# Kernel tuning notes

Measured on AMD Instinct MI355X. Metric: run time of the kernel, lower is better.

Reference implementation:

```python
import jax, jax.numpy as jnp
import numpy as np

N, E, D_IN, D_E, H, OUT, L = 16384, 131072, 128, 64, 256, 16, 4
EPS_MSG = 1e-7   # GENConv message epsilon
EPS_SM = 1e-16   # PyG softmax denominator epsilon


def _ln(x, g, b, eps=1e-5):
    mu = x.mean(-1, keepdims=True)
    var = x.var(-1, keepdims=True)
    return (x - mu) * jax.lax.rsqrt(var + eps) * g + b


def _genconv(x, src, dst, e, w1, b1, lng, lnb, w2, b2, t):
    # message: relu(x_j + edge_attr) + eps  -> [E, H]
    msg = jax.nn.relu(x[src] + e) + EPS_MSG
    # learnable-temperature segment softmax over incoming edges, per feature
    m = msg * t
    mx = jax.ops.segment_max(m, dst, num_segments=N)
    mx = jnp.where(jnp.isfinite(mx), mx, 0.0)  # empty segments -> 0
    ex = jnp.exp(m - mx[dst])
    den = jax.ops.segment_sum(ex, dst, num_segments=N)
    alpha = ex / (den[dst] + EPS_SM)
    agg = jax.ops.segment_sum(msg * alpha, dst, num_segments=N)  # [N, H]
    # root residual then 2-layer MLP: Linear -> LayerNorm -> ReLU -> Linear
    out = agg + x
    h = jax.nn.relu(_ln(out @ w1 + b1, lng, lnb))
    return h @ w2 + b2


def setup_inputs() -> dict:
    key = jax.random.key(0)
    ks = jax.random.split(key, 10)
    gl = lambda k, shape, fan: jax.random.normal(k, shape, jnp.float32) / np.sqrt(fan).astype(np.float32)
    return {
        "x": jax.random.normal(ks[0], (N, D_IN), jnp.float32),
        "edge_index": jax.random.randint(ks[1], (2, E), 0, N, dtype=jnp.int32),
        "edge_attr": jax.random.normal(ks[2], (E, D_E), jnp.float32),
        "enc_w": gl(ks[3], (D_IN, H), D_IN), "enc_b": jnp.zeros((H,), jnp.float32),
        "ee_w": gl(ks[4], (D_E, H), D_E), "ee_b": jnp.zeros((H,), jnp.float32),
        "w1": gl(ks[5], (L, H, 2 * H), H), "b1": jnp.zeros((L, 2 * H), jnp.float32),
        "lng": jnp.ones((L, 2 * H), jnp.float32), "lnb": jnp.zeros((L, 2 * H), jnp.float32),
        "w2": gl(ks[6], (L, 2 * H, H), 2 * H), "b2": jnp.zeros((L, H), jnp.float32),
        "t": jnp.ones((L,), jnp.float32),
        "ng": jnp.ones((L, H), jnp.float32), "nb": jnp.zeros((L, H), jnp.float32),
        "lin_w": gl(ks[7], (H, OUT), H), "lin_b": jnp.zeros((OUT,), jnp.float32),
    }


def reference(x, edge_index, edge_attr, enc_w, enc_b, ee_w, ee_b,
              w1, b1, lng, lnb, w2, b2, t, ng, nb, lin_w, lin_b):
    src, dst = edge_index[0], edge_index[1]
    h = x @ enc_w + enc_b                      # node encoder
    e = edge_attr @ ee_w + ee_b                # edge encoder
    # first layer: conv only (per source forward)
    h = _genconv(h, src, dst, e, w1[0], b1[0], lng[0], lnb[0], w2[0], b2[0], t[0])
    # remaining layers: res+ block = x + conv(relu(norm(x)))  (dropout off in eval)
    for i in range(1, L):
        z = jax.nn.relu(_ln(h, ng[i], nb[i]))
        h = h + _genconv(z, src, dst, e, w1[i], b1[i], lng[i], lnb[i], w2[i], b2[i], t[i])
    h = jax.nn.relu(_ln(h, ng[0], nb[0]))      # layers[0].act(layers[0].norm(x))
    return h @ lin_w + lin_b
```

## Files before the change

kernel.cpp:

```cpp
#include <hip/hip_runtime.h>
#include <stdint.h>
#include <math.h>


typedef __bf16 bf16x8 __attribute__((ext_vector_type(8)));
typedef __bf16 bf16x4 __attribute__((ext_vector_type(4)));
typedef float  f32x4  __attribute__((ext_vector_type(4)));

constexpr int NN   = 16384;
constexpr int NE   = 131072;
constexpr int DIN  = 128;
constexpr int DE   = 64;
constexpr int HD   = 256;
constexpr int HD2  = 512;

__device__ __forceinline__ void gl_lds16(const __bf16* g, __bf16* l) {
  __builtin_amdgcn_global_load_lds((const __attribute__((address_space(1))) void*)g,
                                   (__attribute__((address_space(3))) void*)l, 16, 0, 0);
}

__global__ __launch_bounds__(1024) void k_scan(const int* __restrict__ deg,
                                               int* __restrict__ row_start) {
  __shared__ int part[1024];
  const int t = threadIdx.x;
  const int base = t * 16;
  int loc[16];
  int s = 0;
  #pragma unroll
  for (int i = 0; i < 16; i++) { loc[i] = s; s += deg[base + i]; }
  part[t] = s;
  __syncthreads();
  for (int off = 1; off < 1024; off <<= 1) {
    int v = (t >= off) ? part[t - off] : 0;
    __syncthreads();
    part[t] += v;
    __syncthreads();
  }
  const int excl = (t == 0) ? 0 : part[t - 1];
  #pragma unroll
  for (int i = 0; i < 16; i++) row_start[base + i] = excl + loc[i];
}

__global__ void k_scatter(const int* __restrict__ src, const int* __restrict__ dst,
                          const int* __restrict__ row_start, int* __restrict__ cursor,
                          int2* __restrict__ csr_es) {
  int e = blockIdx.x * 256 + threadIdx.x;
  if (e >= NE) return;
  const int d = dst[e];
  const int p = atomicAdd(&cursor[d], 1);
  csr_es[row_start[d] + p] = make_int2(e, src[e]);
}

__global__ __launch_bounds__(256)
void k_sortw(const int* __restrict__ row_start, const int* __restrict__ deg,
             int2* __restrict__ csr_es, int* __restrict__ posmap) {
  const int wv   = threadIdx.x >> 6;
  const int lane = threadIdx.x & 63;
  const int node = blockIdx.x * 4 + wv;
  if (node >= NN) return;
  const int st = __builtin_amdgcn_readfirstlane(row_start[node]);
  const int dg = __builtin_amdgcn_readfirstlane(deg[node]);
  if (dg <= 1) {
    if (dg == 1 && lane == 0) posmap[csr_es[st].x] = st;
    return;
  }
  if (dg <= 64) {
    int2 pr = make_int2(0x7fffffff, 0);
    if (lane < dg) pr = csr_es[st + lane];
    int rank = 0;
    for (int j = 0; j < dg; j++) {
      const int ej = __builtin_amdgcn_readlane(pr.x, j);
      if (lane < dg && ej < pr.x) rank++;
    }
    if (lane < dg) {
      csr_es[st + rank] = pr;
      posmap[pr.x] = st + rank;
    }
  } else if (lane == 0) {
    for (int a = 1; a < dg; a++) {
      int2 k = csr_es[st + a];
      int b = a - 1;
      while (b >= 0 && csr_es[st + b].x > k.x) { csr_es[st + b + 1] = csr_es[st + b]; b--; }
      csr_es[st + b + 1] = k;
    }
    for (int a = 0; a < dg; a++) posmap[csr_es[st + a].x] = st + a;
  }
}

__global__ void k_prep(const float* __restrict__ enc_w, const float* __restrict__ ee_w,
                       const float* __restrict__ w1, const float* __restrict__ w2,
                       const int* __restrict__ dst, int* __restrict__ deg,
                       __bf16* __restrict__ enc_wT, __bf16* __restrict__ ee_wT,
                       __bf16* __restrict__ w1T, __bf16* __restrict__ w2T) {
  int i = blockIdx.x * 256 + threadIdx.x;
  const int S0 = DIN * HD, S1 = DE * HD, S2 = 4 * HD * HD2, S3 = 4 * HD2 * HD;
  if (i < S0) { int k = i / HD, n = i % HD; enc_wT[n * DIN + k] = (__bf16)enc_w[i]; return; }
  i -= S0;
  if (i < S1) { int k = i / HD, n = i % HD; ee_wT[n * DE + k] = (__bf16)ee_w[i]; return; }
  i -= S1;
  if (i < S2) {
    int l = i / (HD * HD2), r = i % (HD * HD2), k = r / HD2, n = r % HD2;
    w1T[(size_t)l * HD * HD2 + (size_t)n * HD + k] = (__bf16)w1[i]; return;
  }
  i -= S2;
  if (i < S3) {
    int l = i / (HD2 * HD), r = i % (HD2 * HD), k = r / HD, n = r % HD;
    w2T[(size_t)l * HD2 * HD + (size_t)n * HD2 + k] = (__bf16)w2[i]; return;
  }
  i -= S3;
  if (i < NE) { atomicAdd(&deg[dst[i]], 1); return; }
}

template <int RES, int OBF, int STATS, int ESCAT, int AF32>
__global__ __launch_bounds__(256, 3)
void k_gemm(const void* __restrict__ Ap, const __bf16* __restrict__ BT,
            const float* __restrict__ bias, const float* __restrict__ R,
            float* __restrict__ Cf, __bf16* __restrict__ Cb,
            const int* __restrict__ posmap, float2* __restrict__ pstats,
            int M, int Nn, int K) {
  __shared__ __attribute__((aligned(16))) char smem[49152];
  float (*sm)[129] = (float(*)[129])smem;
  float* sbias     = (float*)(smem + 16512);
  float2 (*pst4)[32] = (float2(*)[32])(smem + 17024);
  const __bf16* Ab = (const __bf16*)Ap;
  const float*  Af = (const float*)Ap;
  const int tid  = threadIdx.x;
  const int lane = tid & 63;
  const int wave = tid >> 6;
  const int ntn  = Nn >> 7;
  const int bid  = (int)blockIdx.x;
  const int bn   = (bid >> 3) % ntn;
  const int bm   = (bid & 7) + ((bid >> 3) / ntn) * 8;
  const size_t row0 = (size_t)bm * 128, col0 = (size_t)bn * 128;
  const int wr = (wave >> 1) * 64, wc = (wave & 1) * 64;
  const int ks = lane >> 4, fr = lane & 15;

  auto bufA = [&](int i) -> __bf16* { return (__bf16*)(smem + i * 8192); };
  auto bufB = [&](int i) -> __bf16* { return (__bf16*)(smem + 24576 + i * 8192); };

  f32x4 acc[4][4] = {};

  const int arow = tid >> 2;
  const int aksg = (tid & 3) ^ ((arow >> 1) & 3);

  auto stageB = [&](__bf16* lb, int k0) {
    gl_lds16(BT + (col0 + arow) * K + k0 + aksg * 8, &lb[tid * 8]);
    gl_lds16(BT + (col0 + arow + 64) * K + k0 + aksg * 8, &lb[(tid + 256) * 8]);
  };
  auto stageA = [&](__bf16* la, int k0) {
    gl_lds16(Ab + (row0 + arow) * K + k0 + aksg * 8, &la[tid * 8]);
    gl_lds16(Ab + (row0 + arow + 64) * K + k0 + aksg * 8, &la[(tid + 256) * 8]);
  };
  float4 p0, p1, q0, q1;
  auto loadAf = [&](int k0) {
    const float* a0p = &Af[(row0 + arow) * K + k0 + aksg * 8];
    const float* a1p = &Af[(row0 + arow + 64) * K + k0 + aksg * 8];
    p0 = *(const float4*)a0p; p1 = *(const float4*)(a0p + 4);
    q0 = *(const float4*)a1p; q1 = *(const float4*)(a1p + 4);
  };
  auto writeAf = [&](__bf16* la) {
    bf16x8 o0, o1;
    o0[0] = (__bf16)p0.x; o0[1] = (__bf16)p0.y; o0[2] = (__bf16)p0.z; o0[3] = (__bf16)p0.w;
    o0[4] = (__bf16)p1.x; o0[5] = (__bf16)p1.y; o0[6] = (__bf16)p1.z; o0[7] = (__bf16)p1.w;
    o1[0] = (__bf16)q0.x; o1[1] = (__bf16)q0.y; o1[2] = (__bf16)q0.z; o1[3] = (__bf16)q0.w;
    o1[4] = (__bf16)q1.x; o1[5] = (__bf16)q1.y; o1[6] = (__bf16)q1.z; o1[7] = (__bf16)q1.w;
    *(bf16x8*)&la[tid * 8] = o0;
    *(bf16x8*)&la[(tid + 256) * 8] = o1;
  };

  int slA[4], slB[4];
  #pragma unroll
  for (int m = 0; m < 4; m++) {
    const int rm = wr + m * 16 + fr;
    slA[m] = rm * 4 + (ks ^ ((rm >> 1) & 3));
    const int cn = wc + m * 16 + fr;
    slB[m] = cn * 4 + (ks ^ ((cn >> 1) & 3));
  }

  const int nk = K / 32;
  if (AF32) { loadAf(0); stageB(bufB(0), 0); writeAf(bufA(0)); }
  else      { stageA(bufA(0), 0); stageB(bufB(0), 0); }
  if (nk > 1) {
    if (AF32) { loadAf(32); stageB(bufB(1), 32); writeAf(bufA(1)); }
    else      { stageA(bufA(1), 32); stageB(bufB(1), 32); }
  }
  for (int t = 0; t < nk; t++) {
    const int rem = nk - 1 - t;
    const int nb3 = (t + 2) % 3;
    if (rem >= 2) {
      if (AF32) { loadAf((t + 2) * 32); stageB(bufB(nb3), (t + 2) * 32); }
      else      { stageA(bufA(nb3), (t + 2) * 32); stageB(bufB(nb3), (t + 2) * 32); }
    }
    if (AF32) {
      if (rem >= 2)      asm volatile("s_waitcnt vmcnt(8) lgkmcnt(0)" ::: "memory");
      else if (rem == 1) asm volatile("s_waitcnt vmcnt(2) lgkmcnt(0)" ::: "memory");
      else               asm volatile("s_waitcnt vmcnt(0) lgkmcnt(0)" ::: "memory");
    } else {
      if (rem >= 2)      asm volatile("s_waitcnt vmcnt(8)" ::: "memory");
      else if (rem == 1) asm volatile("s_waitcnt vmcnt(4)" ::: "memory");
      else               asm volatile("s_waitcnt vmcnt(0)" ::: "memory");
    }
    __builtin_amdgcn_s_barrier();
    __builtin_amdgcn_sched_barrier(0);
    const __bf16* la = bufA(t % 3);
    const __bf16* lb = bufB(t % 3);
    bf16x8 af[4], bfr[4];
    #pragma unroll
    for (int m = 0; m < 4; m++) af[m]  = *(const bf16x8*)&la[slA[m] * 8];
    #pragma unroll
    for (int n = 0; n < 4; n++) bfr[n] = *(const bf16x8*)&lb[slB[n] * 8];
    #pragma unroll
    for (int m = 0; m < 4; m++)
      #pragma unroll
      for (int n = 0; n < 4; n++)
        acc[m][n] = __builtin_amdgcn_mfma_f32_16x16x32_bf16(af[m], bfr[n], acc[m][n], 0, 0, 0);
    if (AF32 && rem >= 2) writeAf(bufA(nb3));
    __builtin_amdgcn_s_barrier();
  }
  __syncthreads();

  if (tid < 128) sbias[tid] = bias[col0 + tid];
  const int rbase = (wave >> 1) * 16 + ks * 4;
  const int rr = tid >> 3, cs = (tid & 7) * 16;
  #pragma unroll
  for (int m = 0; m < 4; m++) {
    if (m) __syncthreads();
    #pragma unroll
    for (int n = 0; n < 4; n++)
      #pragma unroll
      for (int r = 0; r < 4; r++)
        sm[rbase + r][wc + n * 16 + fr] = acc[m][n][r];
    __syncthreads();
    const size_t lrow = ((rr & 16) ? 64 : 0) + m * 16 + (rr & 15);
    const size_t grow = row0 + lrow;
    float v[16];
    #pragma unroll
    for (int j = 0; j < 16; j++) v[j] = sm[rr][cs + j] + sbias[cs + j];
    if (STATS) {
      float ssum = 0.f, ssq = 0.f;
      #pragma unroll
      for (int j = 0; j < 16; j++) { ssum += v[j]; ssq += v[j] * v[j]; }
      #pragma unroll
      for (int o = 1; o < 8; o <<= 1) {
        ssum += __shfl_xor(ssum, o);
        ssq  += __shfl_xor(ssq, o);
      }
      if ((tid & 7) == 0) pst4[m][rr].x = ssum, pst4[m][rr].y = ssq;
    }
    const size_t gbase = grow * Nn + col0 + cs;
    if (RES) {
      #pragma unroll
      for (int j = 0; j < 16; j += 4) {
        const float4 rv = *(const float4*)&R[gbase + j];
        v[j] += rv.x; v[j + 1] += rv.y; v[j + 2] += rv.z; v[j + 3] += rv.w;
      }
    }
    if (OBF == 0 || OBF == 2) {
      #pragma unroll
      for (int j = 0; j < 16; j += 4) {
        float4 o; o.x = v[j]; o.y = v[j + 1]; o.z = v[j + 2]; o.w = v[j + 3];
        *(float4*)&Cf[gbase + j] = o;
      }
    }
    if (OBF == 1 || OBF == 2) {
      const size_t crow = ESCAT ? (size_t)posmap[grow] : grow;
      const size_t cbase = crow * Nn + col0 + cs;
      bf16x8 o0, o1;
      #pragma unroll
      for (int j = 0; j < 8; j++) { o0[j] = (__bf16)v[j]; o1[j] = (__bf16)v[8 + j]; }
      *(bf16x8*)&Cb[cbase] = o0;
      *(bf16x8*)&Cb[cbase + 8] = o1;
    }
  }
  if (STATS) {
    __syncthreads();
    if (tid < 128) {
      const int lr = tid;
      const int hi = lr >> 6, m2 = (lr >> 4) & 3, rl = lr & 15;
      pstats[(row0 + lr) * ntn + bn] = pst4[m2][(hi << 4) | rl];
    }
  }
}

template <int RES, int WH>
__global__ __launch_bounds__(256, 2)
void k_mlp(const __bf16* __restrict__ a1, const __bf16* __restrict__ w1T,
           const float* __restrict__ b1v, const float* __restrict__ g1,
           const float* __restrict__ bln1, const __bf16* __restrict__ w2T,
           const float* __restrict__ b2v, const float* __restrict__ R,
           const float* __restrict__ g2, const float* __restrict__ bln2,
           float* __restrict__ hout, __bf16* __restrict__ zout) {
  __shared__ __attribute__((aligned(16))) char smem[60928];
  float* sg1    = (float*)smem;
  float* sb1    = (float*)(smem + 2048);
  float* sbias1 = (float*)(smem + 4096);
  float* sg2    = (float*)(smem + 6144);
  float* sb2    = (float*)(smem + 7168);
  float* sbias2 = (float*)(smem + 8192);
  float2* wred  = (float2*)(smem + 9216);
  float2* lnrow = (float2*)(smem + 10240);
  __bf16* a1t   = (__bf16*)(smem + 10496);
  __bf16* a2t   = (__bf16*)(smem + 26880);
  float (*sm)[264] = (float(*)[264])(smem + 26880);

  const int tid = threadIdx.x, lane = tid & 63, wave = tid >> 6;
  const size_t row0 = (size_t)blockIdx.x * 32;
  const int ks = lane >> 4, fr = lane & 15;

  sg1[tid] = g1[tid];     sg1[tid + 256] = g1[tid + 256];
  sb1[tid] = bln1[tid];   sb1[tid + 256] = bln1[tid + 256];
  sbias1[tid] = b1v[tid]; sbias1[tid + 256] = b1v[tid + 256];
  sg2[tid] = g2[tid]; sb2[tid] = bln2[tid]; sbias2[tid] = b2v[tid];

  #pragma unroll
  for (int j = 0; j < 4; j++) {
    const int s = j * 256 + tid;
    const int r = s >> 5;
    const int cl = (s & 31) ^ (r & 31);
    gl_lds16(a1 + (row0 + r) * HD + cl * 8, &a1t[s * 8]);
  }
  __syncthreads();

  f32x4 acc1[2][8] = {};
  {
    auto loadB1 = [&](int t, bf16x8* b) {
      const int k0 = t * 32;
      #pragma unroll
      for (int n = 0; n < 8; n++) {
        const int col = wave * 128 + n * 16 + fr;
        b[n] = *(const bf16x8*)&w1T[(size_t)col * HD + k0 + ks * 8];
      }
    };
    bf16x8 bA[8], bB[8];
    loadB1(0, bA);
    #pragma unroll
    for (int t = 0; t < 8; t++) {
      bf16x8* bc = (t & 1) ? bB : bA;
      bf16x8* bn = (t & 1) ? bA : bB;
      if (t + 1 < 8) loadB1(t + 1, bn);
      bf16x8 af[2];
      #pragma unroll
      for (int m = 0; m < 2; m++) {
        const int rm = m * 16 + fr;
        af[m] = *(const bf16x8*)&a1t[(rm * 32 + ((4 * t + ks) ^ (rm & 31))) * 8];
      }
      #pragma unroll
      for (int m = 0; m < 2; m++)
        #pragma unroll
        for (int n = 0; n < 8; n++)
          acc1[m][n] = __builtin_amdgcn_mfma_f32_16x16x32_bf16(af[m], bc[n], acc1[m][n], 0, 0, 0);
    }
  }
  #pragma unroll
  for (int m = 0; m < 2; m++)
    #pragma unroll
    for (int n = 0; n < 8; n++) {
      const int col = wave * 128 + n * 16 + fr;
      const float bv = sbias1[col];
      #pragma unroll
      for (int r = 0; r < 4; r++) acc1[m][n][r] += bv;
    }
  #pragma unroll
  for (int m = 0; m < 2; m++)
    #pragma unroll
    for (int r = 0; r < 4; r++) {
      float s = 0.f, q = 0.f;
      #pragma unroll
      for (int n = 0; n < 8; n++) { const float v = acc1[m][n][r]; s += v; q += v * v; }
      #pragma unroll
      for (int o = 1; o < 16; o <<= 1) { s += __shfl_xor(s, o); q += __shfl_xor(q, o); }
      if (fr == 0) {
        const int row = m * 16 + ks * 4 + r;
        wred[wave * 32 + row].x = s;
        wred[wave * 32 + row].y = q;
      }
    }
  __syncthreads();
  if (tid < 32) {
    float s = 0.f, q = 0.f;
    #pragma unroll
    for (int w = 0; w < 4; w++) { s += wred[w * 32 + tid].x; q += wred[w * 32 + tid].y; }
    const float mu = s * (1.f / HD2);
    lnrow[tid].x = mu;
    lnrow[tid].y = rsqrtf(q * (1.f / HD2) - mu * mu + 1e-5f);
  }
  __syncthreads();
  #pragma unroll
  for (int m = 0; m < 2; m++)
    #pragma unroll
    for (int r = 0; r < 4; r++) {
      const int row = m * 16 + ks * 4 + r;
      const float mu = lnrow[row].x, iv = lnrow[row].y;
      #pragma unroll
      for (int n = 0; n < 8; n++) {
        const int col = wave * 128 + n * 16 + fr;
        const float f = (acc1[m][n][r] - mu) * iv * sg1[col] + sb1[col];
        const int chunk = col >> 3, sub = col & 7;
        a2t[(row * 64 + (chunk ^ (row & 63))) * 8 + sub] = (__bf16)fmaxf(f, 0.f);
      }
    }
  __syncthreads();

  f32x4 acc2[2][4] = {};
  {
    auto loadB2 = [&](int t, bf16x8* b) {
      const int k0 = t * 32;
      #pragma unroll
      for (int n = 0; n < 4; n++) {
        const int col = wave * 64 + n * 16 + fr;
        b[n] = *(const bf16x8*)&w2T[(size_t)col * HD2 + k0 + ks * 8];
      }
    };
    bf16x8 bA[4], bB[4];
    loadB2(0, bA);
    #pragma unroll
    for (int t = 0; t < 16; t++) {
      bf16x8* bc = (t & 1) ? bB : bA;
      bf16x8* bn = (t & 1) ? bA : bB;
      if (t + 1 < 16) loadB2(t + 1, bn);
      bf16x8 af[2];
      #pragma unroll
      for (int m = 0; m < 2; m++) {
        const int rm = m * 16 + fr;
        af[m] = *(const bf16x8*)&a2t[(rm * 64 + ((4 * t + ks) ^ (rm & 63))) * 8];
      }
      #pragma unroll
      for (int m = 0; m < 2; m++)
        #pragma unroll
        for (int n = 0; n < 4; n++)
          acc2[m][n] = __builtin_amdgcn_mfma_f32_16x16x32_bf16(af[m], bc[n], acc2[m][n], 0, 0, 0);
    }
  }
  __syncthreads();

  #pragma unroll
  for (int m = 0; m < 2; m++)
    #pragma unroll
    for (int n = 0; n < 4; n++)
      #pragma unroll
      for (int r = 0; r < 4; r++)
        sm[m * 16 + ks * 4 + r][wave * 64 + n * 16 + fr] = acc2[m][n][r];
  __syncthreads();
  const int rr = tid >> 3, c0 = (tid & 7) * 4;
  float v[32];
  float s = 0.f, sq = 0.f;
  #pragma unroll
  for (int j = 0; j < 8; j++) {
    const int c = c0 + j * 32;
    float x0 = sm[rr][c]     + sbias2[c];
    float x1 = sm[rr][c + 1] + sbias2[c + 1];
    float x2 = sm[rr][c + 2] + sbias2[c + 2];
    float x3 = sm[rr][c + 3] + sbias2[c + 3];
    if (RES) {
      const float4 rv = *(const float4*)&R[(row0 + rr) * HD + c];
      x0 += rv.x; x1 += rv.y; x2 += rv.z; x3 += rv.w;
    }
    v[j * 4] = x0; v[j * 4 + 1] = x1; v[j * 4 + 2] = x2; v[j * 4 + 3] = x3;
    s += x0 + x1 + x2 + x3;
    sq += x0 * x0 + x1 * x1 + x2 * x2 + x3 * x3;
  }
  #pragma unroll
  for (int o = 1; o < 8; o <<= 1) { s += __shfl_xor(s, o); sq += __shfl_xor(sq, o); }
  const float mu = s * (1.f / HD);
  const float inv = rsqrtf(sq * (1.f / HD) - mu * mu + 1e-5f);
  #pragma unroll
  for (int j = 0; j < 8; j++) {
    const int c = c0 + j * 32;
    if (WH) {
      float4 o;
      o.x = v[j * 4]; o.y = v[j * 4 + 1]; o.z = v[j * 4 + 2]; o.w = v[j * 4 + 3];
      *(float4*)&hout[(row0 + rr) * HD + c] = o;
    }
    bf16x4 z;
    z[0] = (__bf16)fmaxf((v[j * 4]     - mu) * inv * sg2[c]     + sb2[c],     0.f);
    z[1] = (__bf16)fmaxf((v[j * 4 + 1] - mu) * inv * sg2[c + 1] + sb2[c + 1], 0.f);
    z[2] = (__bf16)fmaxf((v[j * 4 + 2] - mu) * inv * sg2[c + 2] + sb2[c + 2], 0.f);
    z[3] = (__bf16)fmaxf((v[j * 4 + 3] - mu) * inv * sg2[c + 3] + sb2[c + 3], 0.f);
    *(bf16x4*)&zout[(row0 + rr) * HD + c] = z;
  }
}

__global__ __launch_bounds__(256)
void k_msg(const __bf16* __restrict__ zb, const __bf16* __restrict__ ecsr,
           const int* __restrict__ row_start, const int* __restrict__ deg,
           const int2* __restrict__ csr_es, const float* __restrict__ tvec,
           int layer, __bf16* __restrict__ a1) {
  const int wv   = __builtin_amdgcn_readfirstlane(threadIdx.x >> 6);
  const int lane = threadIdx.x & 63;
  const int node = blockIdx.x * 4 + wv;
  const int st = __builtin_amdgcn_readfirstlane(row_start[node]);
  const int dg = __builtin_amdgcn_readfirstlane(deg[node]);
  const float t = tvec[layer];
  const int f0 = lane * 4;

  int my_src = 0;
  if (lane < dg) my_src = csr_es[st + lane].y;
  const bf16x4 sv = *(const bf16x4*)&zb[(size_t)node * HD + f0];

  float den[4] = {0.f, 0.f, 0.f, 0.f}, agg[4] = {0.f, 0.f, 0.f, 0.f};
  const int dmain = dg < 64 ? dg : 64;
  int j = 0;
  for (; j + 8 <= dmain; j += 8) {
    bf16x4 zv[8], ev[8];
    #pragma unroll
    for (int u = 0; u < 8; u++) {
      const int sn = __builtin_amdgcn_readlane(my_src, j + u);
      zv[u] = *(const bf16x4*)&zb[(size_t)sn * HD + f0];
      ev[u] = *(const bf16x4*)&ecsr[(size_t)(st + j + u) * HD + f0];
    }
    #pragma unroll
    for (int u = 0; u < 8; u++)
      #pragma unroll
      for (int q = 0; q < 4; q++) {
        const float m  = fmaxf((float)zv[u][q] + (float)ev[u][q], 0.f) + 1e-7f;
        const float ex = __expf(m * t);
        den[q] += ex;
        agg[q] += m * ex;
      }
  }
  for (; j + 4 <= dmain; j += 4) {
    bf16x4 zv[4], ev[4];
    #pragma unroll
    for (int u = 0; u < 4; u++) {
      const int sn = __builtin_amdgcn_readlane(my_src, j + u);
      zv[u] = *(const bf16x4*)&zb[(size_t)sn * HD + f0];
      ev[u] = *(const bf16x4*)&ecsr[(size_t)(st + j + u) * HD + f0];
    }
    #pragma unroll
    for (int u = 0; u < 4; u++)
      #pragma unroll
      for (int q = 0; q < 4; q++) {
        const float m  = fmaxf((float)zv[u][q] + (float)ev[u][q], 0.f) + 1e-7f;
        const float ex = __expf(m * t);
        den[q] += ex;
        agg[q] += m * ex;
      }
  }
  for (; j < dmain; j++) {
    const int sn = __builtin_amdgcn_readlane(my_src, j);
    const bf16x4 zv = *(const bf16x4*)&zb[(size_t)sn * HD + f0];
    const bf16x4 ev = *(const bf16x4*)&ecsr[(size_t)(st + j) * HD + f0];
    #pragma unroll
    for (int q = 0; q < 4; q++) {
      const float m  = fmaxf((float)zv[q] + (float)ev[q], 0.f) + 1e-7f;
      const float ex = __expf(m * t);
      den[q] += ex;
      agg[q] += m * ex;
    }
  }
  for (int jj = 64; jj < dg; jj++) {
    const int2 pr = csr_es[st + jj];
    const bf16x4 zv = *(const bf16x4*)&zb[(size_t)pr.y * HD + f0];
    const bf16x4 ev = *(const bf16x4*)&ecsr[(size_t)(st + jj) * HD + f0];
    #pragma unroll
    for (int q = 0; q < 4; q++) {
      const float m  = fmaxf((float)zv[q] + (float)ev[q], 0.f) + 1e-7f;
      const float ex = __expf(m * t);
      den[q] += ex;
      agg[q] += m * ex;
    }
  }
  bf16x4 r;
  #pragma unroll
  for (int q = 0; q < 4; q++) {
    const float res = (dg > 0) ? agg[q] / (den[q] + 1e-16f) : 0.f;
    r[q] = (__bf16)(res + (float)sv[q]);
  }
  *(bf16x4*)&a1[(size_t)node * HD + f0] = r;
}

__global__ __launch_bounds__(256)
void k_head(const __bf16* __restrict__ zb, const float* __restrict__ lw,
            const float* __restrict__ lb, float* __restrict__ out) {
  __shared__ float slw[256 * 16];
  __shared__ __bf16 srow[16 * 256];
  const int t = threadIdx.x;
  const size_t row0 = (size_t)blockIdx.x * 16;
  #pragma unroll
  for (int j = 0; j < 16; j++) slw[j * 256 + t] = lw[j * 256 + t];
  #pragma unroll
  for (int j = 0; j < 2; j++) {
    const int c = j * 256 + t;
    ((bf16x8*)srow)[c] = ((const bf16x8*)(zb + row0 * 256))[c];
  }
  __syncthreads();
  const int rl = t >> 4, col = t & 15;
  float s = lb[col];
  for (int k0 = 0; k0 < 256; k0 += 8) {
    const bf16x8 zv = *(const bf16x8*)&srow[rl * 256 + k0];
    #pragma unroll
    for (int q = 0; q < 8; q++) s += (float)zv[q] * slw[(k0 + q) * 16 + col];
  }
  out[(row0 + rl) * 16 + col] = s;
}

extern "C" void kernel_launch(void* const* d_in, const int* in_sizes, int n_in,
                              void* d_out, int out_size, void* d_ws, size_t ws_size,
                              hipStream_t stream) {
  const float* x     = (const float*)d_in[0];
  const int*   ei    = (const int*)d_in[1];
  const float* ea    = (const float*)d_in[2];
  const float* enc_w = (const float*)d_in[3];
  const float* enc_b = (const float*)d_in[4];
  const float* ee_w  = (const float*)d_in[5];
  const float* ee_b  = (const float*)d_in[6];
  const float* w1    = (const float*)d_in[7];
  const float* b1    = (const float*)d_in[8];
  const float* lng   = (const float*)d_in[9];
  const float* lnb   = (const float*)d_in[10];
  const float* w2    = (const float*)d_in[11];
  const float* b2    = (const float*)d_in[12];
  const float* tvec  = (const float*)d_in[13];
  const float* ng    = (const float*)d_in[14];
  const float* nb    = (const float*)d_in[15];
  const float* lin_w = (const float*)d_in[16];
  const float* lin_b = (const float*)d_in[17];

  uint8_t* p = (uint8_t*)d_ws;
  auto alloc = [&](size_t bytes) { uint8_t* r = p; p += (bytes + 255) & ~(size_t)255; return r; };
  __bf16* e_csr  = (__bf16*)alloc((size_t)NE * HD * 2);
  float*  h      = (float*) alloc((size_t)NN * HD * 4);
  __bf16* hb     = (__bf16*)alloc((size_t)NN * HD * 2);
  __bf16* zb     = (__bf16*)alloc((size_t)NN * HD * 2);
  __bf16* a1     = (__bf16*)alloc((size_t)NN * HD * 2);
  __bf16* enc_wT = (__bf16*)alloc((size_t)HD * DIN * 2);
  __bf16* ee_wT  = (__bf16*)alloc((size_t)HD * DE * 2);
  __bf16* w1T    = (__bf16*)alloc((size_t)4 * HD2 * HD * 2);
  __bf16* w2T    = (__bf16*)alloc((size_t)4 * HD * HD2 * 2);
  int* deg       = (int*)alloc((size_t)NN * 4);
  int* cursor    = (int*)alloc((size_t)NN * 4);
  int* row_start = (int*)alloc((size_t)NN * 4);
  int* posmap    = (int*)alloc((size_t)NE * 4);
  int2* csr_es   = (int2*)alloc((size_t)NE * 8);

  const int* srcp = ei;
  const int* dstp = ei + NE;

  hipMemsetAsync(deg, 0, (size_t)NN * 8, stream);

  const int prep_total = DIN * HD + DE * HD + 4 * HD * HD2 + 4 * HD2 * HD + NE;
  k_prep<<<(prep_total + 255) / 256, 256, 0, stream>>>(enc_w, ee_w, w1, w2, dstp, deg,
                                                       enc_wT, ee_wT, w1T, w2T);
  k_scan<<<1, 1024, 0, stream>>>(deg, row_start);
  k_scatter<<<NE / 256, 256, 0, stream>>>(srcp, dstp, row_start, cursor, csr_es);
  k_sortw<<<NN / 4, 256, 0, stream>>>(row_start, deg, csr_es, posmap);

  k_gemm<0, 2, 0, 0, 1><<<(NN / 128) * (HD / 128), 256, 0, stream>>>(
      x, enc_wT, enc_b, nullptr, h, hb, nullptr, nullptr, NN, HD, DIN);
  k_gemm<0, 1, 0, 1, 1><<<(NE / 128) * (HD / 128), 256, 0, stream>>>(
      ea, ee_wT, ee_b, nullptr, nullptr, e_csr, posmap, nullptr, NE, HD, DE);

  for (int i = 0; i < 4; i++) {
    const __bf16* zin = (i == 0) ? hb : zb;
    k_msg<<<NN / 4, 256, 0, stream>>>(zin, e_csr, row_start, deg, csr_es, tvec, i, a1);
    const int nidx = (i < 3) ? i + 1 : 0;
    const float* gg = ng + (size_t)nidx * HD;
    const float* bb = nb + (size_t)nidx * HD;
    if (i == 0)
      k_mlp<0, 1><<<NN / 32, 256, 0, stream>>>(
          a1, w1T + (size_t)i * HD2 * HD, b1 + (size_t)i * HD2,
          lng + (size_t)i * HD2, lnb + (size_t)i * HD2,
          w2T + (size_t)i * HD * HD2, b2 + (size_t)i * HD,
          nullptr, gg, bb, h, zb);
    else if (i < 3)
      k_mlp<1, 1><<<NN / 32, 256, 0, stream>>>(
          a1, w1T + (size_t)i * HD2 * HD, b1 + (size_t)i * HD2,
          lng + (size_t)i * HD2, lnb + (size_t)i * HD2,
          w2T + (size_t)i * HD * HD2, b2 + (size_t)i * HD,
          h, gg, bb, h, zb);
    else
      k_mlp<1, 0><<<NN / 32, 256, 0, stream>>>(
          a1, w1T + (size_t)i * HD2 * HD, b1 + (size_t)i * HD2,
          lng + (size_t)i * HD2, lnb + (size_t)i * HD2,
          w2T + (size_t)i * HD * HD2, b2 + (size_t)i * HD,
          h, gg, bb, h, zb);
  }

  k_head<<<NN / 16, 256, 0, stream>>>(zb, lin_w, lin_b, (float*)d_out);
}
```

Baseline: 324.3 us.

## Swap MFMA operand roles in fused MLP kernel and drop GEMM row-stat epilogue

The fused MLP kernel now treats weights as the A operand and node rows as the B operand of the MFMA, so each lane holds four consecutive features of one node. This lets the LayerNorm reductions and the epilogues run directly from registers, with no LDS staging of the input tile or the output tile, and LDS use shrinks. Activations are read straight from global memory instead of through async LDS copies, which risks more redundant global traffic across waves. The STATS partial row-statistics path is also removed from the generic GEMM epilogue.

```diff
diff --git a/kernel.cpp b/kernel.cpp
--- a/kernel.cpp
+++ b/kernel.cpp
@@ -121,7 +121,6 @@
   __shared__ __attribute__((aligned(16))) char smem[49152];
   float (*sm)[129] = (float(*)[129])smem;
   float* sbias     = (float*)(smem + 16512);
-  float2 (*pst4)[32] = (float2(*)[32])(smem + 17024);
   const __bf16* Ab = (const __bf16*)Ap;
   const float*  Af = (const float*)Ap;
   const int tid  = threadIdx.x;
@@ -236,17 +235,6 @@
     float v[16];
     #pragma unroll
     for (int j = 0; j < 16; j++) v[j] = sm[rr][cs + j] + sbias[cs + j];
-    if (STATS) {
-      float ssum = 0.f, ssq = 0.f;
-      #pragma unroll
-      for (int j = 0; j < 16; j++) { ssum += v[j]; ssq += v[j] * v[j]; }
-      #pragma unroll
-      for (int o = 1; o < 8; o <<= 1) {
-        ssum += __shfl_xor(ssum, o);
-        ssq  += __shfl_xor(ssq, o);
-      }
-      if ((tid & 7) == 0) pst4[m][rr].x = ssum, pst4[m][rr].y = ssq;
-    }
     const size_t gbase = grow * Nn + col0 + cs;
     if (RES) {
       #pragma unroll
@@ -270,14 +258,6 @@
       for (int j = 0; j < 8; j++) { o0[j] = (__bf16)v[j]; o1[j] = (__bf16)v[8 + j]; }
       *(bf16x8*)&Cb[cbase] = o0;
       *(bf16x8*)&Cb[cbase + 8] = o1;
-    }
-  }
-  if (STATS) {
-    __syncthreads();
-    if (tid < 128) {
-      const int lr = tid;
-      const int hi = lr >> 6, m2 = (lr >> 4) & 3, rl = lr & 15;
-      pstats[(row0 + lr) * ntn + bn] = pst4[m2][(hi << 4) | rl];
     }
   }
 }
@@ -290,18 +270,16 @@
            const float* __restrict__ b2v, const float* __restrict__ R,
            const float* __restrict__ g2, const float* __restrict__ bln2,
            float* __restrict__ hout, __bf16* __restrict__ zout) {
-  __shared__ __attribute__((aligned(16))) char smem[60928];
-  float* sg1    = (float*)smem;
-  float* sb1    = (float*)(smem + 2048);
-  float* sbias1 = (float*)(smem + 4096);
-  float* sg2    = (float*)(smem + 6144);
-  float* sb2    = (float*)(smem + 7168);
-  float* sbias2 = (float*)(smem + 8192);
-  float2* wred  = (float2*)(smem + 9216);
-  float2* lnrow = (float2*)(smem + 10240);
-  __bf16* a1t   = (__bf16*)(smem + 10496);
-  __bf16* a2t   = (__bf16*)(smem + 26880);
-  float (*sm)[264] = (float(*)[264])(smem + 26880);
+  __shared__ __attribute__((aligned(16))) char smem[43264];
+  float*  sg1    = (float*)smem;
+  float*  sb1    = (float*)(smem + 2048);
+  float*  sbias1 = (float*)(smem + 4096);
+  float*  sg2    = (float*)(smem + 6144);
+  float*  sb2    = (float*)(smem + 7168);
+  float*  sbias2 = (float*)(smem + 8192);
+  float2* wred   = (float2*)(smem + 9216);
+  float2* lnrow  = (float2*)(smem + 10240);
+  __bf16* a2s    = (__bf16*)(smem + 10496);
 
   const int tid = threadIdx.x, lane = tid & 63, wave = tid >> 6;
   const size_t row0 = (size_t)blockIdx.x * 32;
@@ -311,172 +289,163 @@
   sb1[tid] = bln1[tid];   sb1[tid + 256] = bln1[tid + 256];
   sbias1[tid] = b1v[tid]; sbias1[tid + 256] = b1v[tid + 256];
   sg2[tid] = g2[tid]; sb2[tid] = bln2[tid]; sbias2[tid] = b2v[tid];
-
-  #pragma unroll
-  for (int j = 0; j < 4; j++) {
-    const int s = j * 256 + tid;
-    const int r = s >> 5;
-    const int cl = (s & 31) ^ (r & 31);
-    gl_lds16(a1 + (row0 + r) * HD + cl * 8, &a1t[s * 8]);
-  }
-  __syncthreads();
-
-  f32x4 acc1[2][8] = {};
+  __syncthreads();
+
+  f32x4 acc1[8][2] = {};
+  #pragma unroll
+  for (int t = 0; t < 8; t++) {
+    bf16x8 af[8], bfr[2];
+    #pragma unroll
+    for (int mi = 0; mi < 8; mi++)
+      af[mi] = *(const bf16x8*)&w1T[(size_t)(wave * 128 + mi * 16 + fr) * HD + t * 32 + ks * 8];
+    #pragma unroll
+    for (int nt = 0; nt < 2; nt++)
+      bfr[nt] = *(const bf16x8*)&a1[(row0 + nt * 16 + fr) * HD + t * 32 + ks * 8];
+    #pragma unroll
+    for (int mi = 0; mi < 8; mi++)
+      #pragma unroll
+      for (int nt = 0; nt < 2; nt++)
+        acc1[mi][nt] = __builtin_amdgcn_mfma_f32_16x16x32_bf16(af[mi], bfr[nt], acc1[mi][nt], 0, 0, 0);
+  }
+
   {
-    auto loadB1 = [&](int t, bf16x8* b) {
-      const int k0 = t * 32;
-      #pragma unroll
-      for (int n = 0; n < 8; n++) {
-        const int col = wave * 128 + n * 16 + fr;
-        b[n] = *(const bf16x8*)&w1T[(size_t)col * HD + k0 + ks * 8];
-      }
-    };
-    bf16x8 bA[8], bB[8];
-    loadB1(0, bA);
-    #pragma unroll
-    for (int t = 0; t < 8; t++) {
-      bf16x8* bc = (t & 1) ? bB : bA;
-      bf16x8* bn = (t & 1) ? bA : bB;
-      if (t + 1 < 8) loadB1(t + 1, bn);
-      bf16x8 af[2];
-      #pragma unroll
-      for (int m = 0; m < 2; m++) {
-        const int rm = m * 16 + fr;
-        af[m] = *(const bf16x8*)&a1t[(rm * 32 + ((4 * t + ks) ^ (rm & 31))) * 8];
-      }
-      #pragma unroll
-      for (int m = 0; m < 2; m++)
+    float s[2] = {0.f, 0.f}, q[2] = {0.f, 0.f};
+    #pragma unroll
+    for (int mi = 0; mi < 8; mi++)
+      #pragma unroll
+      for (int r = 0; r < 4; r++) {
+        const int f = wave * 128 + mi * 16 + ks * 4 + r;
+        const float bv = sbias1[f];
         #pragma unroll
-        for (int n = 0; n < 8; n++)
-          acc1[m][n] = __builtin_amdgcn_mfma_f32_16x16x32_bf16(af[m], bc[n], acc1[m][n], 0, 0, 0);
-    }
-  }
-  #pragma unroll
-  for (int m = 0; m < 2; m++)
-    #pragma unroll
-    for (int n = 0; n < 8; n++) {
-      const int col = wave * 128 + n * 16 + fr;
-      const float bv = sbias1[col];
-      #pragma unroll
-      for (int r = 0; r < 4; r++) acc1[m][n][r] += bv;
-    }
-  #pragma unroll
-  for (int m = 0; m < 2; m++)
-    #pragma unroll
-    for (int r = 0; r < 4; r++) {
-      float s = 0.f, q = 0.f;
-      #pragma unroll
-      for (int n = 0; n < 8; n++) { const float v = acc1[m][n][r]; s += v; q += v * v; }
-      #pragma unroll
-      for (int o = 1; o < 16; o <<= 1) { s += __shfl_xor(s, o); q += __shfl_xor(q, o); }
-      if (fr == 0) {
-        const int row = m * 16 + ks * 4 + r;
-        wred[wave * 32 + row].x = s;
-        wred[wave * 32 + row].y = q;
-      }
-    }
+        for (int nt = 0; nt < 2; nt++) {
+          const float v = acc1[mi][nt][r] + bv;
+          acc1[mi][nt][r] = v;
+          s[nt] += v; q[nt] += v * v;
+        }
+      }
+    #pragma unroll
+    for (int nt = 0; nt < 2; nt++) {
+      s[nt] += __shfl_xor(s[nt], 16); q[nt] += __shfl_xor(q[nt], 16);
+      s[nt] += __shfl_xor(s[nt], 32); q[nt] += __shfl_xor(q[nt], 32);
+    }
+    if (lane < 16) {
+      wred[wave * 32 + fr].x = s[0];      wred[wave * 32 + fr].y = q[0];
+      wred[wave * 32 + 16 + fr].x = s[1]; wred[wave * 32 + 16 + fr].y = q[1];
+    }
+  }
   __syncthreads();
   if (tid < 32) {
-    float s = 0.f, q = 0.f;
-    #pragma unroll
-    for (int w = 0; w < 4; w++) { s += wred[w * 32 + tid].x; q += wred[w * 32 + tid].y; }
-    const float mu = s * (1.f / HD2);
+    float ss = 0.f, qq = 0.f;
+    #pragma unroll
+    for (int w = 0; w < 4; w++) { ss += wred[w * 32 + tid].x; qq += wred[w * 32 + tid].y; }
+    const float mu = ss * (1.f / HD2);
     lnrow[tid].x = mu;
-    lnrow[tid].y = rsqrtf(q * (1.f / HD2) - mu * mu + 1e-5f);
-  }
-  __syncthreads();
-  #pragma unroll
-  for (int m = 0; m < 2; m++)
-    #pragma unroll
-    for (int r = 0; r < 4; r++) {
-      const int row = m * 16 + ks * 4 + r;
-      const float mu = lnrow[row].x, iv = lnrow[row].y;
-      #pragma unroll
-      for (int n = 0; n < 8; n++) {
-        const int col = wave * 128 + n * 16 + fr;
-        const float f = (acc1[m][n][r] - mu) * iv * sg1[col] + sb1[col];
-        const int chunk = col >> 3, sub = col & 7;
-        a2t[(row * 64 + (chunk ^ (row & 63))) * 8 + sub] = (__bf16)fmaxf(f, 0.f);
-      }
-    }
-  __syncthreads();
-
-  f32x4 acc2[2][4] = {};
+    lnrow[tid].y = rsqrtf(qq * (1.f / HD2) - mu * mu + 1e-5f);
+  }
+  __syncthreads();
+
+  #pragma unroll
+  for (int nt = 0; nt < 2; nt++) {
+    const int node = nt * 16 + fr;
+    const float mu = lnrow[node].x, iv = lnrow[node].y;
+    #pragma unroll
+    for (int mi = 0; mi < 8; mi++) {
+      const int cc = wave * 32 + mi * 4 + ks;
+      bf16x4 o;
+      #pragma unroll
+      for (int r = 0; r < 4; r++) {
+        const int f = cc * 4 + r;
+        o[r] = (__bf16)fmaxf((acc1[mi][nt][r] - mu) * iv * sg1[f] + sb1[f], 0.f);
+      }
+      *(bf16x4*)&a2s[(node * 128 + (cc ^ node)) * 4] = o;
+    }
+  }
+  __syncthreads();
+
+  f32x4 acc2[4][2] = {};
+  #pragma unroll
+  for (int t = 0; t < 16; t++) {
+    bf16x8 af[4], bfr[2];
+    #pragma unroll
+    for (int mi = 0; mi < 4; mi++)
+      af[mi] = *(const bf16x8*)&w2T[(size_t)(wave * 64 + mi * 16 + fr) * HD2 + t * 32 + ks * 8];
+    #pragma unroll
+    for (int nt = 0; nt < 2; nt++) {
+      const int node = nt * 16 + fr;
+      const int kc = t * 8 + ks * 2;
+      const bf16x4 lo = *(const bf16x4*)&a2s[(node * 128 + (kc ^ node)) * 4];
+      const bf16x4 hi = *(const bf16x4*)&a2s[(node * 128 + ((kc + 1) ^ node)) * 4];
+      bf16x8 b;
+      b[0] = lo[0]; b[1] = lo[1]; b[2] = lo[2]; b[3] = lo[3];
+      b[4] = hi[0]; b[5] = hi[1]; b[6] = hi[2]; b[7] = hi[3];
+      bfr[nt] = b;
+    }
+    #pragma unroll
+    for (int mi = 0; mi < 4; mi++)
+      #pragma unroll
+      for (int nt = 0; nt < 2; nt++)
+        acc2[mi][nt] = __builtin_amdgcn_mfma_f32_16x16x32_bf16(af[mi], bfr[nt], acc2[mi][nt], 0, 0, 0);
+  }
+  __syncthreads();
+
   {
-    auto loadB2 = [&](int t, bf16x8* b) {
-      const int k0 = t * 32;
-      #pragma unroll
-      for (int n = 0; n < 4; n++) {
-        const int col = wave * 64 + n * 16 + fr;
-        b[n] = *(const bf16x8*)&w2T[(size_t)col * HD2 + k0 + ks * 8];
-      }
-    };
-    bf16x8 bA[4], bB[4];
-    loadB2(0, bA);
-    #pragma unroll
-    for (int t = 0; t < 16; t++) {
-      bf16x8* bc = (t & 1) ? bB : bA;
-      bf16x8* bn = (t & 1) ? bA : bB;
-      if (t + 1 < 16) loadB2(t + 1, bn);
-      bf16x8 af[2];
-      #pragma unroll
-      for (int m = 0; m < 2; m++) {
-        const int rm = m * 16 + fr;
-        af[m] = *(const bf16x8*)&a2t[(rm * 64 + ((4 * t + ks) ^ (rm & 63))) * 8];
-      }
-      #pragma unroll
-      for (int m = 0; m < 2; m++)
+    float s[2] = {0.f, 0.f}, q[2] = {0.f, 0.f};
+    #pragma unroll
+    for (int nt = 0; nt < 2; nt++) {
+      const int node = nt * 16 + fr;
+      #pragma unroll
+      for (int mi = 0; mi < 4; mi++) {
+        const int f0 = wave * 64 + mi * 16 + ks * 4;
+        float4 rv;
+        if (RES) rv = *(const float4*)&R[(row0 + node) * HD + f0];
         #pragma unroll
-        for (int n = 0; n < 4; n++)
-          acc2[m][n] = __builtin_amdgcn_mfma_f32_16x16x32_bf16(af[m], bc[n], acc2[m][n], 0, 0, 0);
-    }
-  }
-  __syncthreads();
-
-  #pragma unroll
-  for (int m = 0; m < 2; m++)
-    #pragma unroll
-    for (int n = 0; n < 4; n++)
+        for (int r = 0; r < 4; r++) {
+          float v = acc2[mi][nt][r] + sbias2[f0 + r];
+          if (RES) v += (r == 0) ? rv.x : (r == 1) ? rv.y : (r == 2) ? rv.z : rv.w;
+          acc2[mi][nt][r] = v;
+          s[nt] += v; q[nt] += v * v;
+        }
+      }
+    }
+    #pragma unroll
+    for (int nt = 0; nt < 2; nt++) {
+      s[nt] += __shfl_xor(s[nt], 16); q[nt] += __shfl_xor(q[nt], 16);
+      s[nt] += __shfl_xor(s[nt], 32); q[nt] += __shfl_xor(q[nt], 32);
+    }
+    if (lane < 16) {
+      wred[wave * 32 + fr].x = s[0];      wred[wave * 32 + fr].y = q[0];
+      wred[wave * 32 + 16 + fr].x = s[1]; wred[wave * 32 + 16 + fr].y = q[1];
+    }
+  }
+  __syncthreads();
+  if (tid < 32) {
+    float ss = 0.f, qq = 0.f;
+    #pragma unroll
+    for (int w = 0; w < 4; w++) { ss += wred[w * 32 + tid].x; qq += wred[w * 32 + tid].y; }
+    const float mu = ss * (1.f / HD);
+    lnrow[tid].x = mu;
+    lnrow[tid].y = rsqrtf(qq * (1.f / HD) - mu * mu + 1e-5f);
+  }
+  __syncthreads();
+  #pragma unroll
+  for (int nt = 0; nt < 2; nt++) {
+    const int node = nt * 16 + fr;
+    const float mu = lnrow[node].x, iv = lnrow[node].y;
+    #pragma unroll
+    for (int mi = 0; mi < 4; mi++) {
+      const int f0 = wave * 64 + mi * 16 + ks * 4;
+      if (WH) {
+        float4 o;
+        o.x = acc2[mi][nt][0]; o.y = acc2[mi][nt][1];
+        o.z = acc2[mi][nt][2]; o.w = acc2[mi][nt][3];
+        *(float4*)&hout[(row0 + node) * HD + f0] = o;
+      }
+      bf16x4 z;
       #pragma unroll
       for (int r = 0; r < 4; r++)
-        sm[m * 16 + ks * 4 + r][wave * 64 + n * 16 + fr] = acc2[m][n][r];
-  __syncthreads();
-  const int rr = tid >> 3, c0 = (tid & 7) * 4;
-  float v[32];
-  float s = 0.f, sq = 0.f;
-  #pragma unroll
-  for (int j = 0; j < 8; j++) {
-    const int c = c0 + j * 32;
-    float x0 = sm[rr][c]     + sbias2[c];
-    float x1 = sm[rr][c + 1] + sbias2[c + 1];
-    float x2 = sm[rr][c + 2] + sbias2[c + 2];
-    float x3 = sm[rr][c + 3] + sbias2[c + 3];
-    if (RES) {
-      const float4 rv = *(const float4*)&R[(row0 + rr) * HD + c];
-      x0 += rv.x; x1 += rv.y; x2 += rv.z; x3 += rv.w;
-    }
-    v[j * 4] = x0; v[j * 4 + 1] = x1; v[j * 4 + 2] = x2; v[j * 4 + 3] = x3;
-    s += x0 + x1 + x2 + x3;
-    sq += x0 * x0 + x1 * x1 + x2 * x2 + x3 * x3;
-  }
-  #pragma unroll
-  for (int o = 1; o < 8; o <<= 1) { s += __shfl_xor(s, o); sq += __shfl_xor(sq, o); }
-  const float mu = s * (1.f / HD);
-  const float inv = rsqrtf(sq * (1.f / HD) - mu * mu + 1e-5f);
-  #pragma unroll
-  for (int j = 0; j < 8; j++) {
-    const int c = c0 + j * 32;
-    if (WH) {
-      float4 o;
-      o.x = v[j * 4]; o.y = v[j * 4 + 1]; o.z = v[j * 4 + 2]; o.w = v[j * 4 + 3];
-      *(float4*)&hout[(row0 + rr) * HD + c] = o;
-    }
-    bf16x4 z;
-    z[0] = (__bf16)fmaxf((v[j * 4]     - mu) * inv * sg2[c]     + sb2[c],     0.f);
-    z[1] = (__bf16)fmaxf((v[j * 4 + 1] - mu) * inv * sg2[c + 1] + sb2[c + 1], 0.f);
-    z[2] = (__bf16)fmaxf((v[j * 4 + 2] - mu) * inv * sg2[c + 2] + sb2[c + 2], 0.f);
-    z[3] = (__bf16)fmaxf((v[j * 4 + 3] - mu) * inv * sg2[c + 3] + sb2[c + 3], 0.f);
-    *(bf16x4*)&zout[(row0 + rr) * HD + c] = z;
+        z[r] = (__bf16)fmaxf((acc2[mi][nt][r] - mu) * iv * sg2[f0 + r] + sb2[f0 + r], 0.f);
+      *(bf16x4*)&zout[(row0 + node) * HD + f0] = z;
+    }
   }
 }
 
```

New measurement: 344.6 us. 6.3% more time.
